# Kernel optimization log

Measured on AMD Instinct MI355X. Metric: run time of the kernel, lower is better.

## Reference

```python
import jax, jax.numpy as jnp
import numpy as np
from jax import lax

CHANNEL = 64
HIDDEN = 128

def _conv(x, w, b):
    # x: [B, Cin, H, W], w: [Cout, Cin, 3, 3] -> [B, Cout, H, W], SAME padding
    y = lax.conv_general_dilated(x, w, window_strides=(1, 1), padding='SAME',
                                 dimension_numbers=('NCHW', 'OIHW', 'NCHW'))
    return y + b[None, :, None, None]

def setup_inputs() -> dict:
    key = jax.random.key(0)
    ks = jax.random.split(key, 5)
    T, B, C, H, W = 12, 2, CHANNEL, 128, 128
    x = jax.random.normal(ks[0], (T, B, C, H, W), dtype=jnp.float32)
    fan_g = (C + HIDDEN) * 9
    W_gates = jax.random.normal(ks[1], (4 * HIDDEN, C + HIDDEN, 3, 3), dtype=jnp.float32) / np.sqrt(fan_g)
    b_gates = jnp.zeros((4 * HIDDEN,), dtype=jnp.float32)
    W_out = jax.random.normal(ks[2], (C, HIDDEN, 3, 3), dtype=jnp.float32) / np.sqrt(HIDDEN * 9)
    b_out = jnp.zeros((C,), dtype=jnp.float32)
    return {'x': x, 'W_gates': W_gates, 'b_gates': b_gates, 'W_out': W_out, 'b_out': b_out}

def _convlstm_forward(x, W_gates, b_gates, W_out, b_out):
    T, B, C, H, W = x.shape
    h0 = jnp.zeros((B, HIDDEN, H, W), dtype=x.dtype)
    c0 = jnp.zeros((B, HIDDEN, H, W), dtype=x.dtype)

    def step(carry, xt):
        h, c = carry
        gates = _conv(jnp.concatenate([xt, h], axis=1), W_gates, b_gates)
        i_g, f_g, o_g, g_g = jnp.split(gates, 4, axis=1)
        c = jax.nn.sigmoid(f_g) * c + jax.nn.sigmoid(i_g) * jnp.tanh(g_g)
        h = jax.nn.sigmoid(o_g) * jnp.tanh(c)
        return (h, c), h

    _, hs = lax.scan(step, (h0, c0), x)          # hs: [T, B, HIDDEN, H, W]
    out = _conv(hs.reshape(T * B, HIDDEN, H, W), W_out, b_out)
    return out.reshape(T, B, C, H, W)

def reference(x, W_gates, b_gates, W_out, b_out):
    return _convlstm_forward(x, W_gates, b_gates, W_out, b_out)
```

## Files before the change

kernel.cpp:

```cpp
#include <hip/hip_runtime.h>

typedef _Float16 f16;
typedef __attribute__((ext_vector_type(8))) _Float16 f16x8;
typedef __attribute__((ext_vector_type(4))) _Float16 f16x4;
typedef __attribute__((ext_vector_type(4))) float f32x4;

#define SLICE_H 4326400


__device__ __forceinline__ void gld_lds16(void* lds, const void* g) {
  __builtin_amdgcn_global_load_lds(
      (const __attribute__((address_space(1))) void*)g,
      (__attribute__((address_space(3))) void*)lds, 16, 0, 0);
}

__device__ __forceinline__ float sigf(float v) { return 1.0f / (1.0f + __expf(-v)); }
__device__ __forceinline__ float tanh_fast(float v) { return 2.0f / (1.0f + __expf(-2.0f * v)) - 1.0f; }


__global__ __launch_bounds__(256) void kwt(const float* __restrict__ wsrc,
                                           f16* __restrict__ th, int R) {
  int idx = blockIdx.x * 256 + threadIdx.x;
  if (idx >= 9 * R) return;
  int tap = idx / R, r = idx - tap * R;
  th[idx] = (f16)wsrc[(size_t)r * 9 + tap];
}


__global__ __launch_bounds__(256) void kxform(const float* __restrict__ xt,
                                              f16* __restrict__ xp) {
  int pid = blockIdx.x * 256 + threadIdx.x;
  int b = pid >> 14, y = (pid >> 7) & 127, x = pid & 127;
  const float* src = xt + (size_t)b * 64 * 16384 + (size_t)y * 128 + x;
  size_t doff = ((size_t)((b * 130 + y + 1) * 130 + (x + 1))) * 64;
#pragma unroll
  for (int cc = 0; cc < 8; ++cc) {
    f16x8 vh;
#pragma unroll
    for (int j = 0; j < 8; ++j) vh[j] = (f16)src[(size_t)(cc * 8 + j) * 16384];
    *(f16x8*)(xp + doff + cc * 8) = vh;
  }
}


#define SMEM_G (25344 + 32768)

__global__ __launch_bounds__(512, 4) void kgates(
    const f16* __restrict__ xp, const f16* __restrict__ hp,
    const f16* __restrict__ wg, f16* __restrict__ gates) {
  extern __shared__ char smem[];
  f16* Ap = (f16*)smem;
  f16* Bp = (f16*)(smem + 25344);
  const int tid = threadIdx.x;
  const int lane = tid & 63;
  const int w = tid >> 6;
  const int y = blockIdx.x;
  const int b = blockIdx.y;
  const int n0 = blockIdx.z * 256;
  const int wm = w >> 2, wn = w & 3;
  const int chunk = (lane & 3) ^ ((lane >> 3) & 3);

  f32x4 acc[4][4] = {};

  auto stageA = [&](int cig) {
    const f16* S; int CS, cigl;
    if (cig < 2) { S = xp; CS = 64;  cigl = cig; }
    else         { S = hp; CS = 128; cigl = cig - 2; }
    for (int i = w; i < 27; i += 8) {
      int dy = i / 9, sub = i - dy * 9;
      int xp0 = sub * 16;
      const f16* src = S +
          ((size_t)((b * 130 + y + dy) * 130 + xp0 + (lane >> 2))) * CS +
          cigl * 32 + chunk * 8;
      f16* dst = Ap + (dy * 132 + xp0) * 32;
      if (sub == 8) { if (lane < 16) gld_lds16(dst, src); }
      else gld_lds16(dst, src);
    }
  };
  auto stageB = [&](int cig, int tap, int buf) {
    for (int i = w; i < 16; i += 8) {
      const f16* src = wg +
          ((size_t)(tap * 512 + n0 + i * 16 + (lane >> 2))) * 192 +
          cig * 32 + chunk * 8;
      gld_lds16(Bp + buf * 8192 + i * 512, src);
    }
  };

  stageA(0);
  stageB(0, 0, 0);
  __syncthreads();

  int pp = 0;
  for (int cig = 0; cig < 6; ++cig) {
    for (int tap = 0; tap < 9; ++tap) {
      if (tap < 8) stageB(cig, tap + 1, pp ^ 1);
      else if (cig < 5) stageB(cig + 1, 0, pp ^ 1);
      const int dy = tap / 3, dx = tap - dy * 3;
      const int q = lane >> 4;
      f16x8 af[4], bfr[4];
#pragma unroll
      for (int mf = 0; mf < 4; ++mf) {
        int r = wm * 64 + mf * 16 + (lane & 15) + dx;
        af[mf] = *(const f16x8*)(Ap + (dy * 132 + r) * 32 + ((q ^ ((r >> 1) & 3)) << 3));
      }
#pragma unroll
      for (int nf = 0; nf < 4; ++nf) {
        int n = wn * 64 + nf * 16 + (lane & 15);
        bfr[nf] = *(const f16x8*)(Bp + pp * 8192 + n * 32 + ((q ^ ((n >> 1) & 3)) << 3));
      }
#pragma unroll
      for (int mf = 0; mf < 4; ++mf)
#pragma unroll
        for (int nf = 0; nf < 4; ++nf)
          acc[mf][nf] = __builtin_amdgcn_mfma_f32_16x16x32_f16(af[mf], bfr[nf], acc[mf][nf], 0, 0, 0);
      __syncthreads();
      pp ^= 1;
    }
    if (cig < 5) { stageA(cig + 1); __syncthreads(); }
  }

  size_t pixbase = ((size_t)(b * 128 + y)) * 128;
#pragma unroll
  for (int mf = 0; mf < 4; ++mf) {
#pragma unroll
    for (int nf = 0; nf < 4; ++nf) {
      int cout = n0 + wn * 64 + nf * 16 + (lane & 15);
#pragma unroll
      for (int r = 0; r < 4; ++r) {
        int x = wm * 64 + mf * 16 + (lane >> 4) * 4 + r;
        gates[(pixbase + x) * 512 + cout] = (f16)acc[mf][nf][r];
      }
    }
  }
}


__global__ __launch_bounds__(256) void kpoint(const f16* __restrict__ gates,
                                              const float* __restrict__ bg,
                                              float* __restrict__ cbuf,
                                              f16* __restrict__ hslot) {
  int gid = blockIdx.x * 256 + threadIdx.x;
  int pixel = gid >> 5, cq = gid & 31;
  int b = pixel >> 14, y = (pixel >> 7) & 127, x = pixel & 127;
  size_t gb = (size_t)pixel * 512 + cq * 4;
  const f16x4 ig = *(const f16x4*)(gates + gb);
  const f16x4 fg = *(const f16x4*)(gates + gb + 128);
  const f16x4 og = *(const f16x4*)(gates + gb + 256);
  const f16x4 gg = *(const f16x4*)(gates + gb + 384);
  const f32x4 bi  = *(const f32x4*)(bg + cq * 4);
  const f32x4 bff = *(const f32x4*)(bg + cq * 4 + 128);
  const f32x4 boo = *(const f32x4*)(bg + cq * 4 + 256);
  const f32x4 bgg = *(const f32x4*)(bg + cq * 4 + 384);
  f32x4 co = *(const f32x4*)(cbuf + (size_t)pixel * 128 + cq * 4);
  f32x4 cn;
  f16x4 hh;
#pragma unroll
  for (int j = 0; j < 4; ++j) {
    float iv = sigf((float)ig[j] + bi[j]);
    float fv = sigf((float)fg[j] + bff[j]);
    float ov = sigf((float)og[j] + boo[j]);
    float gv = tanh_fast((float)gg[j] + bgg[j]);
    float cv = fv * co[j] + iv * gv;
    float hv = ov * tanh_fast(cv);
    cn[j] = cv;
    hh[j] = (f16)hv;
  }
  *(f32x4*)(cbuf + (size_t)pixel * 128 + cq * 4) = cn;
  size_t hoff = ((size_t)((b * 130 + y + 1) * 130 + (x + 1))) * 128 + cq * 4;
  *(f16x4*)(hslot + hoff) = hh;
}


#define SMEM_O (25344 + 8192)

__global__ __launch_bounds__(256, 4) void koutconv(
    const f16* __restrict__ hr, int slot0, const f16* __restrict__ wo,
    const float* __restrict__ bo, float* __restrict__ outb) {
  extern __shared__ char smem[];
  f16* Ap = (f16*)smem;
  f16* Bp = (f16*)(smem + 25344);
  const int tid = threadIdx.x, lane = tid & 63, w = tid >> 6;
  const int y = blockIdx.x;
  const int b = blockIdx.y;
  const int ts = blockIdx.z;
  const f16* hp = hr + (size_t)((slot0 + ts) % 5) * SLICE_H;
  float* outt = outb + (size_t)ts * 2 * 64 * 16384;
  const int chunk = (lane & 3) ^ ((lane >> 3) & 3);

  f32x4 acc[2][4] = {};

  auto stageA = [&](int cig) {
    for (int i = w; i < 27; i += 4) {
      int dy = i / 9, sub = i - dy * 9;
      int xp0 = sub * 16;
      const f16* src = hp +
          ((size_t)((b * 130 + y + dy) * 130 + xp0 + (lane >> 2))) * 128 +
          cig * 32 + chunk * 8;
      f16* dst = Ap + (dy * 132 + xp0) * 32;
      if (sub == 8) { if (lane < 16) gld_lds16(dst, src); }
      else gld_lds16(dst, src);
    }
  };
  auto stageB = [&](int cig, int tap, int buf) {
    const f16* src = wo +
        ((size_t)(tap * 64 + w * 16 + (lane >> 2))) * 128 +
        cig * 32 + chunk * 8;
    gld_lds16(Bp + buf * 2048 + w * 512, src);
  };

  stageA(0);
  stageB(0, 0, 0);
  __syncthreads();

  int pp = 0;
  for (int cig = 0; cig < 4; ++cig) {
    for (int tap = 0; tap < 9; ++tap) {
      if (tap < 8) stageB(cig, tap + 1, pp ^ 1);
      else if (cig < 3) stageB(cig + 1, 0, pp ^ 1);
      const int dy = tap / 3, dx = tap - dy * 3;
      const int q = lane >> 4;
      f16x8 af[2], bfr[4];
#pragma unroll
      for (int mf = 0; mf < 2; ++mf) {
        int r = w * 32 + mf * 16 + (lane & 15) + dx;
        af[mf] = *(const f16x8*)(Ap + (dy * 132 + r) * 32 + ((q ^ ((r >> 1) & 3)) << 3));
      }
#pragma unroll
      for (int nf = 0; nf < 4; ++nf) {
        int n = nf * 16 + (lane & 15);
        bfr[nf] = *(const f16x8*)(Bp + pp * 2048 + n * 32 + ((q ^ ((n >> 1) & 3)) << 3));
      }
#pragma unroll
      for (int mf = 0; mf < 2; ++mf)
#pragma unroll
        for (int nf = 0; nf < 4; ++nf)
          acc[mf][nf] = __builtin_amdgcn_mfma_f32_16x16x32_f16(af[mf], bfr[nf], acc[mf][nf], 0, 0, 0);
      __syncthreads();
      pp ^= 1;
    }
    if (cig < 3) { stageA(cig + 1); __syncthreads(); }
  }

#pragma unroll
  for (int nf = 0; nf < 4; ++nf) {
    int cout = nf * 16 + (lane & 15);
    float bias = bo[cout];
#pragma unroll
    for (int mf = 0; mf < 2; ++mf) {
      int xbase = w * 32 + mf * 16 + (lane >> 4) * 4;
      f32x4 v = acc[mf][nf];
      v[0] += bias; v[1] += bias; v[2] += bias; v[3] += bias;
      *(f32x4*)(outt + (((size_t)b * 64 + cout) * 128 + y) * 128 + xbase) = v;
    }
  }
}


extern "C" void kernel_launch(void* const* d_in, const int* in_sizes, int n_in,
                              void* d_out, int out_size, void* d_ws, size_t ws_size,
                              hipStream_t stream) {
  const float* x  = (const float*)d_in[0];
  const float* Wg = (const float*)d_in[1];
  const float* bg = (const float*)d_in[2];
  const float* Wo = (const float*)d_in[3];
  const float* bo = (const float*)d_in[4];
  float* out = (float*)d_out;

  char* base = (char*)d_ws;
  size_t off = 0;
  auto carve = [&](size_t bytes) {
    char* p = base + off;
    off += (bytes + 1023) & ~(size_t)1023;
    return p;
  };
  const size_t PADPOS = (size_t)2 * 130 * 130;
  const size_t xpad_b  = PADPOS * 64 * 2 + 1024;
  const size_t hring_b = (size_t)5 * SLICE_H * 2 + 1024;
  const size_t c_b = (size_t)2 * 128 * 128 * 128 * 4;
  const size_t g_b = (size_t)2 * 128 * 128 * 512 * 2;

  f16* xp    = (f16*)carve(xpad_b);
  f16* hr    = (f16*)carve(hring_b);
  float* cbuf = (float*)carve(c_b);
  f16* gates = (f16*)carve(g_b);
  f16* wg    = (f16*)carve((size_t)9 * 512 * 192 * 2);
  f16* wo    = (f16*)carve((size_t)9 * 64 * 128 * 2);

  hipMemsetAsync(xp, 0, xpad_b, stream);
  hipMemsetAsync(hr, 0, hring_b, stream);
  hipMemsetAsync(cbuf, 0, c_b, stream);

  kwt<<<(9 * 512 * 192 + 255) / 256, 256, 0, stream>>>(Wg, wg, 512 * 192);
  kwt<<<(9 * 64 * 128 + 255) / 256, 256, 0, stream>>>(Wo, wo, 64 * 128);

  for (int t = 0; t < 12; ++t) {
    const float* xt = x + (size_t)t * 2 * 64 * 16384;
    kxform<<<128, 256, 0, stream>>>(xt, xp);
    kgates<<<dim3(128, 2, 2), 512, SMEM_G, stream>>>(
        xp, hr + (size_t)(t % 5) * SLICE_H, wg, gates);
    kpoint<<<4096, 256, 0, stream>>>(gates, bg, cbuf,
        hr + (size_t)((t + 1) % 5) * SLICE_H);
    if ((t & 3) == 3) {
      koutconv<<<dim3(128, 2, 4), 256, SMEM_O, stream>>>(
          hr, (t - 2) % 5, wo, bo, out + (size_t)(t - 3) * 2 * 64 * 16384);
    }
  }
}
```

Before: 1.144 ms.

## Triple-buffer weight tiles with prefetch distance two and partial vmcnt waits

Both conv kernels now keep three LDS buffers for the weight (B) tiles instead of two. Each tile is prefetched two steps ahead, and the two-level cig/tap loop is flattened into one loop. The full __syncthreads is replaced by explicit s_waitcnt vmcnt(N) plus s_barrier, so a wave waits only for the older loads, and MFMA blocks are wrapped in s_setprio. The aim is to hide global-to-LDS latency for the weights, at the cost of more LDS per block (which may lower occupancy in kgates) and fragile hand-written wait counts.

```diff
diff --git a/kernel.cpp b/kernel.cpp
--- a/kernel.cpp
+++ b/kernel.cpp
@@ -43,14 +43,14 @@
 }
 
 
-#define SMEM_G (25344 + 32768)
+#define SMEM_G (25344 + 49152)
 
 __global__ __launch_bounds__(512, 4) void kgates(
     const f16* __restrict__ xp, const f16* __restrict__ hp,
     const f16* __restrict__ wg, f16* __restrict__ gates) {
   extern __shared__ char smem[];
   f16* Ap = (f16*)smem;
-  f16* Bp = (f16*)(smem + 25344);
+  f16* Br = (f16*)(smem + 25344);
   const int tid = threadIdx.x;
   const int lane = tid & 63;
   const int w = tid >> 6;
@@ -77,46 +77,57 @@
       else gld_lds16(dst, src);
     }
   };
-  auto stageB = [&](int cig, int tap, int buf) {
+  auto stageB = [&](int j) {
+    int cig = j / 9, tap = j - cig * 9;
+    f16* dst = Br + (j % 3) * 8192;
     for (int i = w; i < 16; i += 8) {
       const f16* src = wg +
           ((size_t)(tap * 512 + n0 + i * 16 + (lane >> 2))) * 192 +
           cig * 32 + chunk * 8;
-      gld_lds16(Bp + buf * 8192 + i * 512, src);
+      gld_lds16(dst + i * 512, src);
     }
   };
 
   stageA(0);
-  stageB(0, 0, 0);
-  __syncthreads();
-
-  int pp = 0;
-  for (int cig = 0; cig < 6; ++cig) {
-    for (int tap = 0; tap < 9; ++tap) {
-      if (tap < 8) stageB(cig, tap + 1, pp ^ 1);
-      else if (cig < 5) stageB(cig + 1, 0, pp ^ 1);
-      const int dy = tap / 3, dx = tap - dy * 3;
-      const int q = lane >> 4;
-      f16x8 af[4], bfr[4];
-#pragma unroll
-      for (int mf = 0; mf < 4; ++mf) {
-        int r = wm * 64 + mf * 16 + (lane & 15) + dx;
-        af[mf] = *(const f16x8*)(Ap + (dy * 132 + r) * 32 + ((q ^ ((r >> 1) & 3)) << 3));
-      }
-#pragma unroll
-      for (int nf = 0; nf < 4; ++nf) {
-        int n = wn * 64 + nf * 16 + (lane & 15);
-        bfr[nf] = *(const f16x8*)(Bp + pp * 8192 + n * 32 + ((q ^ ((n >> 1) & 3)) << 3));
-      }
-#pragma unroll
-      for (int mf = 0; mf < 4; ++mf)
-#pragma unroll
-        for (int nf = 0; nf < 4; ++nf)
-          acc[mf][nf] = __builtin_amdgcn_mfma_f32_16x16x32_f16(af[mf], bfr[nf], acc[mf][nf], 0, 0, 0);
-      __syncthreads();
-      pp ^= 1;
-    }
-    if (cig < 5) { stageA(cig + 1); __syncthreads(); }
+  stageB(0);
+  stageB(1);
+  asm volatile("s_waitcnt vmcnt(2)" ::: "memory");
+  __builtin_amdgcn_s_barrier();
+
+  for (int j = 0; j < 54; ++j) {
+    const int cig = j / 9, tap = j - cig * 9;
+    const int dy = tap / 3, dx = tap - dy * 3;
+    const int q = lane >> 4;
+    const f16* Bc = Br + (j % 3) * 8192;
+    f16x8 af[4], bfr[4];
+#pragma unroll
+    for (int mf = 0; mf < 4; ++mf) {
+      int r = wm * 64 + mf * 16 + (lane & 15) + dx;
+      af[mf] = *(const f16x8*)(Ap + (dy * 132 + r) * 32 + ((q ^ ((r >> 1) & 3)) << 3));
+    }
+#pragma unroll
+    for (int nf = 0; nf < 4; ++nf) {
+      int n = wn * 64 + nf * 16 + (lane & 15);
+      bfr[nf] = *(const f16x8*)(Bc + n * 32 + ((q ^ ((n >> 1) & 3)) << 3));
+    }
+    if (j + 2 < 54) stageB(j + 2);
+    __builtin_amdgcn_s_setprio(1);
+#pragma unroll
+    for (int mf = 0; mf < 4; ++mf)
+#pragma unroll
+      for (int nf = 0; nf < 4; ++nf)
+        acc[mf][nf] = __builtin_amdgcn_mfma_f32_16x16x32_f16(af[mf], bfr[nf], acc[mf][nf], 0, 0, 0);
+    __builtin_amdgcn_s_setprio(0);
+    if (tap == 8) {
+      __builtin_amdgcn_s_barrier();
+      if (cig < 5) stageA(cig + 1);
+      asm volatile("s_waitcnt vmcnt(0)" ::: "memory");
+      __builtin_amdgcn_s_barrier();
+    } else {
+      if (j + 2 < 54) asm volatile("s_waitcnt vmcnt(2)" ::: "memory");
+      else            asm volatile("s_waitcnt vmcnt(0)" ::: "memory");
+      __builtin_amdgcn_s_barrier();
+    }
   }
 
   size_t pixbase = ((size_t)(b * 128 + y)) * 128;
@@ -171,14 +182,14 @@
 }
 
 
-#define SMEM_O (25344 + 8192)
+#define SMEM_O (25344 + 12288)
 
 __global__ __launch_bounds__(256, 4) void koutconv(
     const f16* __restrict__ hr, int slot0, const f16* __restrict__ wo,
     const float* __restrict__ bo, float* __restrict__ outb) {
   extern __shared__ char smem[];
   f16* Ap = (f16*)smem;
-  f16* Bp = (f16*)(smem + 25344);
+  f16* Br = (f16*)(smem + 25344);
   const int tid = threadIdx.x, lane = tid & 63, w = tid >> 6;
   const int y = blockIdx.x;
   const int b = blockIdx.y;
@@ -201,44 +212,54 @@
       else gld_lds16(dst, src);
     }
   };
-  auto stageB = [&](int cig, int tap, int buf) {
+  auto stageB = [&](int j) {
+    int cig = j / 9, tap = j - cig * 9;
     const f16* src = wo +
         ((size_t)(tap * 64 + w * 16 + (lane >> 2))) * 128 +
         cig * 32 + chunk * 8;
-    gld_lds16(Bp + buf * 2048 + w * 512, src);
+    gld_lds16(Br + (j % 3) * 2048 + w * 512, src);
   };
 
   stageA(0);
-  stageB(0, 0, 0);
-  __syncthreads();
-
-  int pp = 0;
-  for (int cig = 0; cig < 4; ++cig) {
-    for (int tap = 0; tap < 9; ++tap) {
-      if (tap < 8) stageB(cig, tap + 1, pp ^ 1);
-      else if (cig < 3) stageB(cig + 1, 0, pp ^ 1);
-      const int dy = tap / 3, dx = tap - dy * 3;
-      const int q = lane >> 4;
-      f16x8 af[2], bfr[4];
-#pragma unroll
-      for (int mf = 0; mf < 2; ++mf) {
-        int r = w * 32 + mf * 16 + (lane & 15) + dx;
-        af[mf] = *(const f16x8*)(Ap + (dy * 132 + r) * 32 + ((q ^ ((r >> 1) & 3)) << 3));
-      }
-#pragma unroll
-      for (int nf = 0; nf < 4; ++nf) {
-        int n = nf * 16 + (lane & 15);
-        bfr[nf] = *(const f16x8*)(Bp + pp * 2048 + n * 32 + ((q ^ ((n >> 1) & 3)) << 3));
-      }
-#pragma unroll
-      for (int mf = 0; mf < 2; ++mf)
-#pragma unroll
-        for (int nf = 0; nf < 4; ++nf)
-          acc[mf][nf] = __builtin_amdgcn_mfma_f32_16x16x32_f16(af[mf], bfr[nf], acc[mf][nf], 0, 0, 0);
-      __syncthreads();
-      pp ^= 1;
-    }
-    if (cig < 3) { stageA(cig + 1); __syncthreads(); }
+  stageB(0);
+  stageB(1);
+  asm volatile("s_waitcnt vmcnt(1)" ::: "memory");
+  __builtin_amdgcn_s_barrier();
+
+  for (int j = 0; j < 36; ++j) {
+    const int cig = j / 9, tap = j - cig * 9;
+    const int dy = tap / 3, dx = tap - dy * 3;
+    const int q = lane >> 4;
+    const f16* Bc = Br + (j % 3) * 2048;
+    f16x8 af[2], bfr[4];
+#pragma unroll
+    for (int mf = 0; mf < 2; ++mf) {
+      int r = w * 32 + mf * 16 + (lane & 15) + dx;
+      af[mf] = *(const f16x8*)(Ap + (dy * 132 + r) * 32 + ((q ^ ((r >> 1) & 3)) << 3));
+    }
+#pragma unroll
+    for (int nf = 0; nf < 4; ++nf) {
+      int n = nf * 16 + (lane & 15);
+      bfr[nf] = *(const f16x8*)(Bc + n * 32 + ((q ^ ((n >> 1) & 3)) << 3));
+    }
+    if (j + 2 < 36) stageB(j + 2);
+    __builtin_amdgcn_s_setprio(1);
+#pragma unroll
+    for (int mf = 0; mf < 2; ++mf)
+#pragma unroll
+      for (int nf = 0; nf < 4; ++nf)
+        acc[mf][nf] = __builtin_amdgcn_mfma_f32_16x16x32_f16(af[mf], bfr[nf], acc[mf][nf], 0, 0, 0);
+    __builtin_amdgcn_s_setprio(0);
+    if (tap == 8) {
+      __builtin_amdgcn_s_barrier();
+      if (cig < 3) stageA(cig + 1);
+      asm volatile("s_waitcnt vmcnt(0)" ::: "memory");
+      __builtin_amdgcn_s_barrier();
+    } else {
+      if (j + 2 < 36) asm volatile("s_waitcnt vmcnt(1)" ::: "memory");
+      else            asm volatile("s_waitcnt vmcnt(0)" ::: "memory");
+      __builtin_amdgcn_s_barrier();
+    }
   }
 
 #pragma unroll
```

After: 1.134 ms. No clear change (-0.9%).
